# Performance work log

Hardware: AMD Instinct MI355X
Metric: run time of the kernel (lower is better)

Reference implementation:

```python
import jax, jax.numpy as jnp
import numpy as np

D = 1024
H = 16
N = 4096
D_K = D // H
SCALE = D_K ** 0.5


def setup_inputs() -> dict:
    key = jax.random.key(0)
    k_x, k_w = jax.random.split(key)
    X = jax.random.normal(k_x, (N, D), dtype=jnp.float32)
    # nn.Linear(D, 2*D, bias=False): weight [2D, D], y = X @ W.T
    Wqkv = jax.random.normal(k_w, (2 * D, D), dtype=jnp.float32) * (1.0 / np.sqrt(D))
    return {"X": X, "Wqkv": Wqkv}


def reference(X, Wqkv):
    n = X.shape[0]
    proj = X @ Wqkv.T                      # [N, 2D]
    qk, v = jnp.split(proj, 2, axis=-1)    # each [N, D]
    qk = qk.reshape(n, H, D_K)             # [N, H, d_k]
    v = v.reshape(n, H, D_K)
    s = jnp.einsum('nhd,mhd->hnm', qk, qk) / SCALE  # [H, N, N]
    a = jax.nn.softmax(s, axis=-1)
    ctx = jnp.einsum('hnm,mhd->nhd', a, v).reshape(n, H * D_K)
    return ctx
```

## Files before the change

### kernel.cpp

```cpp
#include <hip/hip_runtime.h>
#include <hip/hip_bf16.h>

#define N_TOK   4096
#define D_MODEL 1024
#define H_HEADS 16
#define DK      64
#define KVB     64
#define QK_PRESCALE 0.42466092f


typedef float  f32x4   __attribute__((ext_vector_type(4)));
typedef float  f32x16  __attribute__((ext_vector_type(16)));
typedef short  bf16x8  __attribute__((ext_vector_type(8)));

__device__ __forceinline__ ushort f2bf(float f) {
  union { float f; unsigned u; } v; v.f = f;
  unsigned u = v.u;
  u += 0x7fffu + ((u >> 16) & 1u);
  return (ushort)(u >> 16);
}

__device__ __forceinline__ unsigned cvt_pk_bf16(float lo, float hi) {
  unsigned r;
  asm("v_cvt_pk_bf16_f32 %0, %1, %2" : "=v"(r) : "v"(lo), "v"(hi));
  return r;
}

__device__ __forceinline__ float exp2_raw(float x) {
  float r;
  asm("v_exp_f32 %0, %1" : "=v"(r) : "v"(x));
  return r;
}

__device__ __forceinline__ void gload_lds16(const void* gsrc, void* ldst) {
  __builtin_amdgcn_global_load_lds(
      (const __attribute__((address_space(1))) unsigned int*)gsrc,
      (__attribute__((address_space(3))) unsigned int*)ldst, 16, 0, 0);
}

__device__ __forceinline__ f32x16 mfma32(bf16x8 a, bf16x8 b, f32x16 c) {
  return __builtin_amdgcn_mfma_f32_32x32x16_bf16(a, b, c, 0, 0, 0);
}

__device__ __forceinline__ void swap32(unsigned &a, unsigned &b) {
  asm("v_permlane32_swap_b32 %0, %1" : "+v"(a), "+v"(b));
}

__global__ __launch_bounds__(256) void cvt_bf16_kernel(
    const float* __restrict__ X, const float* __restrict__ W,
    ushort* __restrict__ Xb, ushort* __restrict__ Wb) {
  const size_t i = (size_t)blockIdx.x * 256 + threadIdx.x;
  const float* s;
  ushort* d;
  size_t off;
  if (i < 524288) { s = X; d = Xb; off = i * 8; }
  else            { s = W; d = Wb; off = (i - 524288) * 8; }
  float4 a = *(const float4*)(s + off);
  float4 b = *(const float4*)(s + off + 4);
  ushort4 lo, hi;
  lo.x = f2bf(a.x); lo.y = f2bf(a.y); lo.z = f2bf(a.z); lo.w = f2bf(a.w);
  hi.x = f2bf(b.x); hi.y = f2bf(b.y); hi.z = f2bf(b.z); hi.w = f2bf(b.w);
  *(ushort4*)(d + off)     = lo;
  *(ushort4*)(d + off + 4) = hi;
}

__global__ __launch_bounds__(256) void qkv_gemm_kernel(
    const ushort* __restrict__ Xb, const ushort* __restrict__ Wb,
    ushort* __restrict__ Qb, ushort* __restrict__ Vt) {
  __shared__ ushort As[2][128][32];
  __shared__ ushort Bs[2][128][32];

  const int tid  = threadIdx.x;
  const int lane = tid & 63;
  const int g    = lane >> 4;
  const int lr   = lane & 15;
  const int wave = tid >> 6;
  const int wr   = (wave >> 1) * 64;
  const int wc   = (wave & 1) * 64;

  const int bid = blockIdx.x;
  const int x   = bid & 7;
  const int i   = bid >> 3;
  const int rb  = (x >> 1) * 8 + (i >> 3);
  const int cb  = (x & 1) * 8 + (i & 7);

  f32x4 acc[4][4] = {};

  const int r0 = tid >> 2;
  const int c0 = (tid & 3) * 8;
  const ushort* xsrc = Xb + (size_t)(rb * 128 + r0) * D_MODEL + c0;
  const ushort* wsrc = Wb + (size_t)(cb * 128 + r0) * D_MODEL + c0;

#define GST(BUF, K0)                                                         \
  {                                                                          \
    gload_lds16(xsrc + (K0), (ushort*)As[BUF] + tid * 8);                    \
    gload_lds16(xsrc + 64 * D_MODEL + (K0), (ushort*)As[BUF] + (tid + 256) * 8); \
    gload_lds16(wsrc + (K0), (ushort*)Bs[BUF] + tid * 8);                    \
    gload_lds16(wsrc + 64 * D_MODEL + (K0), (ushort*)Bs[BUF] + (tid + 256) * 8); \
  }

  GST(0, 0);
  __syncthreads();

  for (int k0 = 0; k0 < D_MODEL; k0 += 32) {
    const int buf = (k0 >> 5) & 1;
    if (k0 + 32 < D_MODEL) GST(buf ^ 1, k0 + 32);

    bf16x8 a[4], b[4];
#pragma unroll
    for (int m = 0; m < 4; ++m) a[m] = *(const bf16x8*)&As[buf][wr + m * 16 + lr][g * 8];
#pragma unroll
    for (int n = 0; n < 4; ++n) b[n] = *(const bf16x8*)&Bs[buf][wc + n * 16 + lr][g * 8];

#pragma unroll
    for (int m = 0; m < 4; ++m)
#pragma unroll
      for (int n = 0; n < 4; ++n)
        acc[m][n] = __builtin_amdgcn_mfma_f32_16x16x32_bf16(a[m], b[n], acc[m][n], 0, 0, 0);
    __syncthreads();
  }

  const int nrow0 = rb * 128 + wr;
  const int jcol0 = cb * 128 + wc;
  if (cb < 8) {
#pragma unroll
    for (int m = 0; m < 4; ++m) {
      const int nn = nrow0 + m * 16 + 4 * g;
#pragma unroll
      for (int n = 0; n < 4; ++n) {
        const int j = jcol0 + n * 16 + lr;
#pragma unroll
        for (int r = 0; r < 4; ++r)
          Qb[(size_t)(nn + r) * D_MODEL + j] = f2bf(acc[m][n][r] * QK_PRESCALE);
      }
    }
  } else {
#pragma unroll
    for (int m = 0; m < 4; ++m) {
      const int nn = nrow0 + m * 16 + 4 * g;
#pragma unroll
      for (int n = 0; n < 4; ++n) {
        const int c = jcol0 - D_MODEL + n * 16 + lr;
        uint2 pv = { cvt_pk_bf16(acc[m][n][0], acc[m][n][1]),
                     cvt_pk_bf16(acc[m][n][2], acc[m][n][3]) };
        *(uint2*)(Vt + (size_t)c * N_TOK + nn) = pv;
      }
    }
  }
}

__global__ __launch_bounds__(256, 4) void attn_kernel(
    const ushort* __restrict__ Qb, const ushort* __restrict__ Vg,
    float* __restrict__ Out) {
  __shared__ ushort Kt[2][64][64];
  __shared__ ushort Vt[2][64][64];

  const int tid  = threadIdx.x;
  const int lane = tid & 63;
  const int l31  = lane & 31;
  const int hi   = lane >> 5;
  const int wave = tid >> 6;

  const int bid = blockIdx.x;
  const int i   = bid >> 3;
  const int h   = (bid & 7) * 2 + (i >> 5);
  const int qbase = (i & 31) * 128 + wave * 32;
  const int nit = N_TOK / KVB;

  bf16x8 qf[4];
  const ushort* qrow = Qb + (size_t)(qbase + l31) * D_MODEL + h * DK;
#pragma unroll
  for (int ks = 0; ks < 4; ++ks)
    qf[ks] = *(const bf16x8*)(qrow + ks * 16 + hi * 8);

  float l_run = 0.f;
  const f32x16 zz = {};
  f32x16 ctx0 = {}, ctx1 = {};

  const int srow = tid >> 3;
  const int scg  = (tid & 7) ^ (srow & 7);
  const ushort* kst = Qb + (size_t)srow * D_MODEL + h * DK + scg * 8;
  const ushort* vst = Vg + (size_t)(h * DK + srow) * N_TOK + scg * 8;

#define STAGE_ADV(BUF)                                                        \
  {                                                                           \
    ushort* kd = (ushort*)Kt[BUF] + (size_t)tid * 8;                          \
    ushort* vd = (ushort*)Vt[BUF] + (size_t)tid * 8;                          \
    gload_lds16(kst, kd);                                                     \
    gload_lds16(kst + 32 * D_MODEL, kd + 2048);                               \
    gload_lds16(vst, vd);                                                     \
    gload_lds16(vst + 32 * N_TOK, vd + 2048);                                 \
    kst += (size_t)KVB * D_MODEL;                                             \
    vst += KVB;                                                               \
  }

#define ATTN_BODY(BUF)                                                        \
  {                                                                           \
    if (stages_left > 0) { STAGE_ADV(BUF ^ 1); --stages_left; }               \
    f32x16 st0 = zz, st1 = zz;                                                \
    __builtin_amdgcn_s_setprio(1);                                            \
    _Pragma("unroll")                                                         \
    for (int ks = 0; ks < 4; ++ks) {                                          \
      bf16x8 kf0 = *(const bf16x8*)&Kt[BUF][l31][((((ks << 1) | hi)) ^ (l31 & 7)) << 3]; \
      bf16x8 kf1 = *(const bf16x8*)&Kt[BUF][32 + l31][((((ks << 1) | hi)) ^ (l31 & 7)) << 3]; \
      st0 = mfma32(kf0, qf[ks], st0);                                         \
      st1 = mfma32(kf1, qf[ks], st1);                                         \
    }                                                                         \
    __builtin_amdgcn_s_setprio(0);                                            \
    float rsb[4];                                                             \
    unsigned pk0[8], pk1[8];                                                  \
    _Pragma("unroll")                                                         \
    for (int b = 0; b < 4; ++b) {                                             \
      float a0 = exp2_raw(st0[4 * b + 0]);                                    \
      float a1 = exp2_raw(st0[4 * b + 1]);                                    \
      float a2 = exp2_raw(st0[4 * b + 2]);                                    \
      float a3 = exp2_raw(st0[4 * b + 3]);                                    \
      float c0 = exp2_raw(st1[4 * b + 0]);                                    \
      float c1 = exp2_raw(st1[4 * b + 1]);                                    \
      float c2 = exp2_raw(st1[4 * b + 2]);                                    \
      float c3 = exp2_raw(st1[4 * b + 3]);                                    \
      rsb[b] = ((a0 + a1) + (a2 + a3)) + ((c0 + c1) + (c2 + c3));             \
      pk0[2 * b]     = cvt_pk_bf16(a0, a1);                                   \
      pk0[2 * b + 1] = cvt_pk_bf16(a2, a3);                                   \
      pk1[2 * b]     = cvt_pk_bf16(c0, c1);                                   \
      pk1[2 * b + 1] = cvt_pk_bf16(c2, c3);                                   \
    }                                                                         \
    l_run += (rsb[0] + rsb[1]) + (rsb[2] + rsb[3]);                           \
    _Pragma("unroll")                                                         \
    for (int kt = 0; kt < 2; ++kt) {                                          \
      _Pragma("unroll")                                                       \
      for (int km = 0; km < 2; ++km) {                                        \
        unsigned u0 = kt ? pk1[4 * km + 0] : pk0[4 * km + 0];                 \
        unsigned u1 = kt ? pk1[4 * km + 1] : pk0[4 * km + 1];                 \
        unsigned u2 = kt ? pk1[4 * km + 2] : pk0[4 * km + 2];                 \
        unsigned u3 = kt ? pk1[4 * km + 3] : pk0[4 * km + 3];                 \
        swap32(u0, u2);                                                       \
        swap32(u1, u3);                                                       \
        union { unsigned u[4]; bf16x8 v; } pf;                                \
        pf.u[0] = u0; pf.u[1] = u1; pf.u[2] = u2; pf.u[3] = u3;               \
        const int ck = (kt << 2) | (km << 1) | hi;                            \
        bf16x8 vf0 = *(const bf16x8*)&Vt[BUF][l31][(ck ^ (l31 & 7)) << 3];    \
        bf16x8 vf1 = *(const bf16x8*)&Vt[BUF][32 + l31][(ck ^ (l31 & 7)) << 3]; \
        __builtin_amdgcn_s_setprio(1);                                        \
        ctx0 = mfma32(vf0, pf.v, ctx0);                                       \
        ctx1 = mfma32(vf1, pf.v, ctx1);                                       \
        __builtin_amdgcn_s_setprio(0);                                        \
      }                                                                       \
    }                                                                         \
    __syncthreads();                                                          \
  }

  int stages_left = nit - 1;
  STAGE_ADV(0);
  __syncthreads();

  for (int it = 0; it < nit; it += 2) {
    ATTN_BODY(0);
    ATTN_BODY(1);
  }

  l_run += __shfl_xor(l_run, 32);

  const float inv = 1.f / l_run;
  float* orow = Out + (size_t)(qbase + l31) * D_MODEL + h * DK;
#pragma unroll
  for (int r = 0; r < 16; ++r) {
    const int d = (r & 3) + 8 * (r >> 2) + 4 * hi;
    orow[d]      = ctx0[r] * inv;
    orow[32 + d] = ctx1[r] * inv;
  }
}

extern "C" void kernel_launch(void* const* d_in, const int* in_sizes, int n_in,
                              void* d_out, int out_size, void* d_ws, size_t ws_size,
                              hipStream_t stream) {
  const float* X = (const float*)d_in[0];
  const float* W = (const float*)d_in[1];
  float* Out = (float*)d_out;

  ushort* Qb = (ushort*)d_ws;
  ushort* Vt = Qb + (size_t)N_TOK * D_MODEL;
  ushort* Xb = Vt + (size_t)N_TOK * D_MODEL;
  ushort* Wb = Xb + (size_t)N_TOK * D_MODEL;

  cvt_bf16_kernel<<<dim3(3072), dim3(256), 0, stream>>>(X, W, Xb, Wb);

  qkv_gemm_kernel<<<dim3(512), dim3(256), 0, stream>>>(Xb, Wb, Qb, Vt);

  attn_kernel<<<dim3(512), dim3(256), 0, stream>>>(Qb, Vt, Out);
}
```

Before: 122.1 us.

## Split attention KV range across two wave groups per block with LDS reduction

Doubles the attention block to 512 threads. Two groups of four waves each process half of the key/value sequence for the same 128 query rows, each with its own double-buffered LDS tiles. At the end, partial context accumulators and row sums are exchanged through shared memory and combined, and each group writes half of the output columns. The aim is more waves in flight and a shorter serial KV loop per wave. The cost is 64KB of LDS per block, which may limit how many blocks fit per CU, plus an extra reduction step. The plain sum of partials is valid only because the kernel applies no running max in its softmax.

```diff
diff --git a/kernel.cpp b/kernel.cpp
--- a/kernel.cpp
+++ b/kernel.cpp
@@ -149,23 +149,29 @@
   }
 }
 
-__global__ __launch_bounds__(256, 4) void attn_kernel(
+__global__ __launch_bounds__(512, 4) void attn_kernel(
     const ushort* __restrict__ Qb, const ushort* __restrict__ Vg,
     float* __restrict__ Out) {
-  __shared__ ushort Kt[2][64][64];
-  __shared__ ushort Vt[2][64][64];
+  __shared__ __align__(16) char smem[65536];
 
   const int tid  = threadIdx.x;
   const int lane = tid & 63;
   const int l31  = lane & 31;
   const int hi   = lane >> 5;
   const int wave = tid >> 6;
+  const int quad = wave >> 2;
+  const int wq   = wave & 3;
+  const int qtid = tid & 255;
 
   const int bid = blockIdx.x;
   const int i   = bid >> 3;
   const int h   = (bid & 7) * 2 + (i >> 5);
-  const int qbase = (i & 31) * 128 + wave * 32;
-  const int nit = N_TOK / KVB;
+  const int qbase = (i & 31) * 128 + wq * 32;
+  const int kvlo  = quad * (N_TOK / 2);
+  const int nit   = (N_TOK / 2) / KVB;
+
+  ushort* KtP = (ushort*)(smem + quad * 32768);
+  ushort* VtP = (ushort*)(smem + quad * 32768 + 16384);
 
   bf16x8 qf[4];
   const ushort* qrow = Qb + (size_t)(qbase + l31) * D_MODEL + h * DK;
@@ -177,15 +183,15 @@
   const f32x16 zz = {};
   f32x16 ctx0 = {}, ctx1 = {};
 
-  const int srow = tid >> 3;
-  const int scg  = (tid & 7) ^ (srow & 7);
-  const ushort* kst = Qb + (size_t)srow * D_MODEL + h * DK + scg * 8;
-  const ushort* vst = Vg + (size_t)(h * DK + srow) * N_TOK + scg * 8;
+  const int srow = qtid >> 3;
+  const int scg  = (qtid & 7) ^ (srow & 7);
+  const ushort* kst = Qb + (size_t)(kvlo + srow) * D_MODEL + h * DK + scg * 8;
+  const ushort* vst = Vg + (size_t)(h * DK + srow) * N_TOK + kvlo + scg * 8;
 
 #define STAGE_ADV(BUF)                                                        \
   {                                                                           \
-    ushort* kd = (ushort*)Kt[BUF] + (size_t)tid * 8;                          \
-    ushort* vd = (ushort*)Vt[BUF] + (size_t)tid * 8;                          \
+    ushort* kd = KtP + (BUF) * 4096 + (size_t)qtid * 8;                       \
+    ushort* vd = VtP + (BUF) * 4096 + (size_t)qtid * 8;                       \
     gload_lds16(kst, kd);                                                     \
     gload_lds16(kst + 32 * D_MODEL, kd + 2048);                               \
     gload_lds16(vst, vd);                                                     \
@@ -201,8 +207,10 @@
     __builtin_amdgcn_s_setprio(1);                                            \
     _Pragma("unroll")                                                         \
     for (int ks = 0; ks < 4; ++ks) {                                          \
-      bf16x8 kf0 = *(const bf16x8*)&Kt[BUF][l31][((((ks << 1) | hi)) ^ (l31 & 7)) << 3]; \
-      bf16x8 kf1 = *(const bf16x8*)&Kt[BUF][32 + l31][((((ks << 1) | hi)) ^ (l31 & 7)) << 3]; \
+      bf16x8 kf0 = *(const bf16x8*)(KtP + (BUF) * 4096 + l31 * 64 +           \
+                                    (((((ks << 1) | hi)) ^ (l31 & 7)) << 3)); \
+      bf16x8 kf1 = *(const bf16x8*)(KtP + (BUF) * 4096 + (32 + l31) * 64 +    \
+                                    (((((ks << 1) | hi)) ^ (l31 & 7)) << 3)); \
       st0 = mfma32(kf0, qf[ks], st0);                                         \
       st1 = mfma32(kf1, qf[ks], st1);                                         \
     }                                                                         \
@@ -239,8 +247,10 @@
         union { unsigned u[4]; bf16x8 v; } pf;                                \
         pf.u[0] = u0; pf.u[1] = u1; pf.u[2] = u2; pf.u[3] = u3;               \
         const int ck = (kt << 2) | (km << 1) | hi;                            \
-        bf16x8 vf0 = *(const bf16x8*)&Vt[BUF][l31][(ck ^ (l31 & 7)) << 3];    \
-        bf16x8 vf1 = *(const bf16x8*)&Vt[BUF][32 + l31][(ck ^ (l31 & 7)) << 3]; \
+        bf16x8 vf0 = *(const bf16x8*)(VtP + (BUF) * 4096 + l31 * 64 +         \
+                                      ((ck ^ (l31 & 7)) << 3));               \
+        bf16x8 vf1 = *(const bf16x8*)(VtP + (BUF) * 4096 + (32 + l31) * 64 +  \
+                                      ((ck ^ (l31 & 7)) << 3));               \
         __builtin_amdgcn_s_setprio(1);                                        \
         ctx0 = mfma32(vf0, pf.v, ctx0);                                       \
         ctx1 = mfma32(vf1, pf.v, ctx1);                                       \
@@ -261,13 +271,36 @@
 
   l_run += __shfl_xor(l_run, 32);
 
-  const float inv = 1.f / l_run;
+  float* exA = (float*)smem;
+  float* exB = (float*)(smem + 16384);
+  float* exL = (float*)(smem + 32768);
+  if (quad == 1) {
+#pragma unroll
+    for (int r = 0; r < 16; ++r) exA[(r * 4 + wq) * 64 + lane] = ctx0[r];
+  } else {
+#pragma unroll
+    for (int r = 0; r < 16; ++r) exB[(r * 4 + wq) * 64 + lane] = ctx1[r];
+  }
+  exL[(quad * 4 + wq) * 64 + lane] = l_run;
+  __syncthreads();
+
+  const float lT  = l_run + exL[((1 - quad) * 4 + wq) * 64 + lane];
+  const float inv = 1.f / lT;
   float* orow = Out + (size_t)(qbase + l31) * D_MODEL + h * DK;
-#pragma unroll
-  for (int r = 0; r < 16; ++r) {
-    const int d = (r & 3) + 8 * (r >> 2) + 4 * hi;
-    orow[d]      = ctx0[r] * inv;
-    orow[32 + d] = ctx1[r] * inv;
+  if (quad == 0) {
+#pragma unroll
+    for (int r = 0; r < 16; ++r) {
+      const float v = ctx0[r] + exA[(r * 4 + wq) * 64 + lane];
+      const int d = (r & 3) + 8 * (r >> 2) + 4 * hi;
+      orow[d] = v * inv;
+    }
+  } else {
+#pragma unroll
+    for (int r = 0; r < 16; ++r) {
+      const float v = ctx1[r] + exB[(r * 4 + wq) * 64 + lane];
+      const int d = (r & 3) + 8 * (r >> 2) + 4 * hi;
+      orow[32 + d] = v * inv;
+    }
   }
 }
 
@@ -287,5 +320,5 @@
 
   qkv_gemm_kernel<<<dim3(512), dim3(256), 0, stream>>>(Xb, Wb, Qb, Vt);
 
-  attn_kernel<<<dim3(512), dim3(256), 0, stream>>>(Qb, Vt, Out);
-}
+  attn_kernel<<<dim3(512), dim3(512), 0, stream>>>(Qb, Vt, Out);
+}
```

Result: slower. 124.8 us (+2.2%).
